# Performance work log

Measured on AMD Instinct MI355X. Metric: run time of the kernel, lower is better.

## Reference

```python
import jax, jax.numpy as jnp
import numpy as np

N_GRAPH = 100000
N_CAND = 10
N_TOTAL = N_GRAPH + N_CAND
F_IN = 128
N_TYPES = 10
E = 6400000


def _p(key, shape, scale=0.05):
    return scale * jax.random.normal(key, shape, dtype=jnp.float32)


def setup_inputs() -> dict:
    key = jax.random.key(0)
    ks = jax.random.split(key, 20)
    x = jax.random.normal(ks[0], (N_GRAPH, F_IN), dtype=jnp.float32)
    candidate_set = jax.random.normal(ks[1], (N_CAND, F_IN), dtype=jnp.float32)
    edge_index = jax.random.randint(ks[2], (2, E), 0, N_GRAPH, dtype=jnp.int64)
    candidate_idx = jnp.arange(N_GRAPH, N_TOTAL, dtype=jnp.int64)  # candidate nodes appended last
    return {
        "x": x, "candidate_set": candidate_set,
        "edge_index": edge_index, "candidate_idx": candidate_idx,
        "W1": _p(ks[3], (F_IN, 16)), "b1": jnp.zeros((16,), jnp.float32),
        "W2": _p(ks[4], (16, 24)), "b2": jnp.zeros((24,), jnp.float32),
        "W3": _p(ks[5], (24, 32)), "b3": jnp.zeros((32,), jnp.float32),
        "Ws1": _p(ks[6], (32, 16)), "bs1": jnp.zeros((16,), jnp.float32),
        "Ws2": _p(ks[7], (16, N_TYPES)), "bs2": jnp.zeros((N_TYPES,), jnp.float32),
        "We1": _p(ks[8], (32, 24)), "be1": jnp.zeros((24,), jnp.float32),
        "We2": _p(ks[9], (24, N_TYPES)), "be2": jnp.zeros((N_TYPES,), jnp.float32),
    }


def _gcn(h, src, dst, W, b, n):
    # GCNConv: x' = D^{-1/2}(A+I)D^{-1/2} X W + b (self-loops added)
    h = h @ W
    deg = jax.ops.segment_sum(jnp.ones(src.shape, h.dtype), dst, num_segments=n) + 1.0
    dinv = jax.lax.rsqrt(deg)
    msg = h[src] * (dinv[src] * dinv[dst])[:, None]
    out = jax.ops.segment_sum(msg, dst, num_segments=n)
    out = out + h * (dinv * dinv)[:, None]  # self-loop term
    return out + b


def relu6(x):
    return jnp.clip(x, 0.0, 6.0)


def reference(x, candidate_set, edge_index, candidate_idx,
              W1, b1, W2, b2, W3, b3,
              Ws1, bs1, Ws2, bs2, We1, be1, We2, be2):
    n = N_TOTAL
    src, dst = edge_index[0], edge_index[1]
    h = jnp.concatenate([x, candidate_set], axis=0)  # [n, F_IN]
    h = _gcn(h, src, dst, W1, b1, n)
    h = _gcn(h, src, dst, W2, b2, n)
    h = _gcn(h, src, dst, W3, b3, n)  # [n, 32]

    start_probs = jax.nn.softmax(relu6(h @ Ws1 + bs1) @ Ws2 + bs2, axis=0)  # [n, T]
    mask = jnp.ones_like(start_probs).at[candidate_idx].set(0.0)
    start_probs = start_probs * mask
    start_probs = jnp.where(start_probs == 0.0, 1e-10, start_probs)
    k1, k2 = jax.random.split(jax.random.key(42))
    start_node = jax.random.categorical(k1, jnp.log(start_probs), axis=-1)  # [n]

    combined = jnp.concatenate([h, h[start_node]], axis=0)  # [2n, 32]
    end_probs = jax.nn.softmax(relu6(combined @ We1 + be1) @ We2 + be2, axis=0)  # [2n, T]
    end_probs = end_probs.at[start_node].set(0.0)
    end_probs = jnp.where(end_probs == 0.0, 1e-10, end_probs)
    end_node = jax.random.categorical(k2, jnp.log(end_probs), axis=-1)  # [2n]
    return (start_node, end_node, start_probs, end_probs)
```

## Files before the change

kernel.cpp:

```cpp
#include <hip/hip_runtime.h>
#include <stdint.h>

constexpr int N_GRAPH = 100000;
constexpr int N_CANDS = 10;
constexpr int NT      = N_GRAPH + N_CANDS;
constexpr int F_IN    = 128;
constexpr int NTYPES  = 10;
constexpr int NE      = 6400000;

constexpr int CB_SHIFT = 9;
constexpr int CB       = 1 << CB_SHIFT;
constexpr int NBK2     = (NT + CB - 1) / CB;
constexpr int SB       = 512;
constexpr int NMAT     = NBK2 * SB;
constexpr int NSCAN_B  = NMAT / 256;
constexpr int TMPENT_CAP = NE + NMAT * 15 + 16;

#define RNG_VARIANT 0

typedef float f4v __attribute__((ext_vector_type(4)));

__device__ __forceinline__ void tf2x32(uint32_t k0, uint32_t k1, uint32_t x0, uint32_t x1,
                                       uint32_t& o0, uint32_t& o1) {
  const uint32_t ks2 = k0 ^ k1 ^ 0x1BD11BDAu;
  uint32_t v0 = x0 + k0, v1 = x1 + k1;
#define TFR(r) { v0 += v1; v1 = (v1 << (r)) | (v1 >> (32 - (r))); v1 ^= v0; }
  TFR(13) TFR(15) TFR(26) TFR(6)
  v0 += k1;  v1 += ks2 + 1u;
  TFR(17) TFR(29) TFR(16) TFR(24)
  v0 += ks2; v1 += k0 + 2u;
  TFR(13) TFR(15) TFR(26) TFR(6)
  v0 += k0;  v1 += k1 + 3u;
  TFR(17) TFR(29) TFR(16) TFR(24)
  v0 += k1;  v1 += ks2 + 4u;
  TFR(13) TFR(15) TFR(26) TFR(6)
  v0 += ks2; v1 += k0 + 5u;
#undef TFR
  o0 = v0; o1 = v1;
}

__device__ __forceinline__ void derive_keys(uint32_t& a0, uint32_t& a1,
                                            uint32_t& b0, uint32_t& b1) {
#if RNG_VARIANT == 2
  uint32_t c0, c1, d0, d1;
  tf2x32(0u, 42u, 0u, 2u, c0, c1);
  tf2x32(0u, 42u, 1u, 3u, d0, d1);
  a0 = c0; a1 = d0; b0 = c1; b1 = d1;
#else
  tf2x32(0u, 42u, 0u, 0u, a0, a1);
  tf2x32(0u, 42u, 0u, 1u, b0, b1);
#endif
}

__device__ __forceinline__ uint32_t rng_bits(uint32_t k0, uint32_t k1,
                                             uint32_t idx, uint32_t total) {
#if RNG_VARIANT == 0
  uint32_t o0, o1; tf2x32(k0, k1, 0u, idx, o0, o1); return o0 ^ o1;
#elif RNG_VARIANT == 1
  uint32_t o0, o1; tf2x32(k0, k1, 0u, idx, o0, o1); return o1;
#else
  uint32_t half = total >> 1; uint32_t o0, o1;
  if (idx < half) { tf2x32(k0, k1, idx, idx + half, o0, o1); return o0; }
  tf2x32(k0, k1, idx - half, idx, o0, o1); return o1;
#endif
}

__device__ __forceinline__ double gumbel_from_bits(uint32_t bits) {
  float uf = __uint_as_float((bits >> 9) | 0x3f800000u) - 1.0f;
  uf = fmaxf(1.17549435e-38f, uf + 1.17549435e-38f);
  return -log(-log((double)uf));
}

__device__ __forceinline__ uint32_t encf(float f) {
  uint32_t u = __float_as_uint(f);
  return u ^ ((u & 0x80000000u) ? 0xFFFFFFFFu : 0x80000000u);
}
__device__ __forceinline__ float decf(uint32_t e) {
  uint32_t u = (e & 0x80000000u) ? (e ^ 0x80000000u) : ~e;
  return __uint_as_float(u);
}

__global__ __launch_bounds__(512) void k_bcount(const int* __restrict__ dst,
                                                int* __restrict__ cntmat,
                                                int* __restrict__ cnt) {
  __shared__ int h[NBK2];
  int tid = threadIdx.x, blk = blockIdx.x;
  for (int b = tid; b < NBK2; b += 512) h[b] = 0;
  __syncthreads();
  int per = (NE + SB - 1) / SB;
  int e0 = blk * per, e1 = min(e0 + per, NE);
  for (int e = e0 + tid; e < e1; e += 512) atomicAdd(&h[dst[e] >> CB_SHIFT], 1);
  __syncthreads();
  for (int b = tid; b < NBK2; b += 512) {
    int c = h[b];
    cntmat[b * SB + blk] = (c + 15) & ~15;
    if (c) atomicAdd(&cnt[b], c);
  }
}

__global__ __launch_bounds__(256) void k_s1(int* __restrict__ cmat, int* __restrict__ partial) {
  __shared__ int sm[256];
  int t = blockIdx.x * 256 + threadIdx.x;
  int v = cmat[t];
  sm[threadIdx.x] = v;
  __syncthreads();
  #pragma unroll
  for (int s = 1; s < 256; s <<= 1) {
    int a = (threadIdx.x >= s) ? sm[threadIdx.x - s] : 0;
    __syncthreads();
    sm[threadIdx.x] += a;
    __syncthreads();
  }
  cmat[t] = sm[threadIdx.x] - v;
  if (threadIdx.x == 255) partial[blockIdx.x] = sm[255];
}

__global__ __launch_bounds__(512) void k_s2(int* __restrict__ partial, int* __restrict__ cmat) {
  __shared__ int sm[512];
  int t = threadIdx.x;
  int v = (t < NSCAN_B) ? partial[t] : 0;
  sm[t] = v;
  __syncthreads();
  #pragma unroll
  for (int s = 1; s < 512; s <<= 1) {
    int a = (t >= s) ? sm[t - s] : 0;
    __syncthreads();
    sm[t] += a;
    __syncthreads();
  }
  if (t < NSCAN_B) partial[t] = sm[t] - v;
  if (t == 511) cmat[NMAT] = sm[511];
}

__global__ __launch_bounds__(256) void k_s3(int* __restrict__ cmat, const int* __restrict__ partial) {
  int t = blockIdx.x * 256 + threadIdx.x;
  cmat[t] += partial[blockIdx.x];
}

__global__ __launch_bounds__(256) void k_rowscan(const int* __restrict__ cnt,
                                                 int* __restrict__ rowbase) {
  __shared__ int sm[256];
  int t = threadIdx.x;
  int v = (t < NBK2) ? cnt[t] : 0;
  sm[t] = v;
  __syncthreads();
  #pragma unroll
  for (int s = 1; s < 256; s <<= 1) {
    int a = (t >= s) ? sm[t - s] : 0;
    __syncthreads();
    sm[t] += a;
    __syncthreads();
  }
  if (t < NBK2) rowbase[t] = sm[t] - v;
}

__global__ __launch_bounds__(512) void k_scatter2(const int* __restrict__ src,
                                                  const int* __restrict__ dst,
                                                  const int* __restrict__ cmat,
                                                  uint32_t* __restrict__ tmpent) {
  __shared__ int lcur[NBK2];
  int tid = threadIdx.x, blk = blockIdx.x;
  for (int b = tid; b < NBK2; b += 512) lcur[b] = cmat[b * SB + blk];
  __syncthreads();
  int per = (NE + SB - 1) / SB;
  int e0 = blk * per, e1 = min(e0 + per, NE);
  for (int e = e0 + tid; e < e1; e += 512) {
    int s = src[e], d = dst[e];
    int b = d >> CB_SHIFT;
    int pos = atomicAdd(&lcur[b], 1);
    tmpent[pos] = (uint32_t)s | ((uint32_t)(d & (CB - 1)) << 17);
  }
  __syncthreads();
  for (int b = tid; b < NBK2; b += 512) {
    int p = lcur[b];
    int end = cmat[b * SB + blk + 1];
    for (; p < end; ++p) tmpent[p] = 0xFFFFFFFFu;
  }
}

__global__ __launch_bounds__(512) void k_place(const uint32_t* __restrict__ tmpent,
                                               const int* __restrict__ cmat,
                                               const int* __restrict__ rowbase,
                                               int* __restrict__ rowptr,
                                               float* __restrict__ dinv,
                                               int* __restrict__ col) {
  __shared__ int sdeg[CB];
  __shared__ int sexc[CB];
  __shared__ int sscan[CB];
  int b = blockIdx.x, tid = threadIdx.x;
  sdeg[tid] = 0;
  __syncthreads();
  int r0 = cmat[b * SB], r1 = cmat[(b + 1) * SB];
  for (int e = r0 + tid; e < r1; e += 512) {
    uint32_t v = tmpent[e];
    if (v != 0xFFFFFFFFu) atomicAdd(&sdeg[v >> 17], 1);
  }
  __syncthreads();
  int d = sdeg[tid];
  sscan[tid] = d;
  __syncthreads();
  #pragma unroll
  for (int s = 1; s < CB; s <<= 1) {
    int v = (tid >= s) ? sscan[tid - s] : 0;
    __syncthreads();
    sscan[tid] += v;
    __syncthreads();
  }
  int rb = rowbase[b];
  int incl = rb + sscan[tid];
  sexc[tid] = incl - d;
  int i = b * CB + tid;
  if (i < NT) {
    rowptr[i + 1] = incl;
    dinv[i] = (float)(1.0 / sqrt((double)(d + 1)));
  }
  if (b == 0 && tid == 0) rowptr[0] = 0;
  __syncthreads();
  for (int e = r0 + tid; e < r1; e += 512) {
    uint32_t v = tmpent[e];
    if (v != 0xFFFFFFFFu) {
      int pos = atomicAdd(&sexc[v >> 17], 1);
      col[pos] = (int)(v & 0x1FFFFu);
    }
  }
}

__global__ __launch_bounds__(256) void k_mm1(const float* __restrict__ x, const float* __restrict__ cand,
                                             const float* __restrict__ W, const float* __restrict__ dinv,
                                             float* __restrict__ zlo, float* __restrict__ zhi) {
  int gid = blockIdx.x * 256 + threadIdx.x;
  if (gid >= NT * 4) return;
  int i = gid >> 2, f4 = gid & 3;
  const float* hr = (i < N_GRAPH) ? (x + (size_t)i * F_IN)
                                  : (cand + (size_t)(i - N_GRAPH) * F_IN);
  const float4* h4 = reinterpret_cast<const float4*>(hr);
  const float4* W4 = reinterpret_cast<const float4*>(W);
  double a0 = 0.0, a1 = 0.0, a2 = 0.0, a3 = 0.0;
  #pragma unroll 8
  for (int q = 0; q < 32; ++q) {
    float4 hv = h4[q];
    float4 w0 = W4[(4 * q + 0) * 4 + f4];
    float4 w1 = W4[(4 * q + 1) * 4 + f4];
    float4 w2 = W4[(4 * q + 2) * 4 + f4];
    float4 w3 = W4[(4 * q + 3) * 4 + f4];
    a0 += (double)hv.x * w0.x + (double)hv.y * w1.x + (double)hv.z * w2.x + (double)hv.w * w3.x;
    a1 += (double)hv.x * w0.y + (double)hv.y * w1.y + (double)hv.z * w2.y + (double)hv.w * w3.y;
    a2 += (double)hv.x * w0.z + (double)hv.y * w1.z + (double)hv.z * w2.z + (double)hv.w * w3.z;
    a3 += (double)hv.x * w0.w + (double)hv.y * w1.w + (double)hv.z * w2.w + (double)hv.w * w3.w;
  }
  double di = (double)dinv[i];
  float4 o;
  o.x = (float)(a0 * di); o.y = (float)(a1 * di);
  o.z = (float)(a2 * di); o.w = (float)(a3 * di);
  if (f4 < 2) reinterpret_cast<float4*>(zlo)[(size_t)i * 2 + f4] = o;
  else        reinterpret_cast<float4*>(zhi)[(size_t)i * 2 + (f4 - 2)] = o;
}

template <bool SQ, bool WITHW, int R>
__global__ __launch_bounds__(2 * R) void k_proph(const int* __restrict__ rowptr,
                                                 const int* __restrict__ col,
                                                 const float* __restrict__ zin,
                                                 const float* __restrict__ win,
                                                 const float* __restrict__ dinv,
                                                 float* __restrict__ zout,
                                                 float* __restrict__ wout,
                                                 float* __restrict__ wsout) {
  int i = blockIdx.x * R + threadIdx.y;
  if (i >= NT) return;
  int fx = threadIdx.x;
  const float4* z4 = reinterpret_cast<const float4*>(zin);
  int e0 = rowptr[i], e1 = rowptr[i + 1];
  double a0 = 0.0, a1 = 0.0, a2 = 0.0, a3 = 0.0, wa = 0.0;
  int e = e0;
  for (; e + 8 <= e1; e += 8) {
    int c0 = __builtin_nontemporal_load(col + e);
    int c1 = __builtin_nontemporal_load(col + e + 1);
    int c2 = __builtin_nontemporal_load(col + e + 2);
    int c3 = __builtin_nontemporal_load(col + e + 3);
    int c4 = __builtin_nontemporal_load(col + e + 4);
    int c5 = __builtin_nontemporal_load(col + e + 5);
    int c6 = __builtin_nontemporal_load(col + e + 6);
    int c7 = __builtin_nontemporal_load(col + e + 7);
    float4 v0 = z4[(size_t)c0 * 2 + fx];
    float4 v1 = z4[(size_t)c1 * 2 + fx];
    float4 v2 = z4[(size_t)c2 * 2 + fx];
    float4 v3 = z4[(size_t)c3 * 2 + fx];
    float4 v4 = z4[(size_t)c4 * 2 + fx];
    float4 v5 = z4[(size_t)c5 * 2 + fx];
    float4 v6 = z4[(size_t)c6 * 2 + fx];
    float4 v7 = z4[(size_t)c7 * 2 + fx];
    if (WITHW && fx == 0) {
      wa += (double)win[c0] + (double)win[c1] + (double)win[c2] + (double)win[c3];
      wa += (double)win[c4] + (double)win[c5] + (double)win[c6] + (double)win[c7];
    }
    a0 += (double)v0.x + (double)v1.x + (double)v2.x + (double)v3.x;
    a1 += (double)v0.y + (double)v1.y + (double)v2.y + (double)v3.y;
    a2 += (double)v0.z + (double)v1.z + (double)v2.z + (double)v3.z;
    a3 += (double)v0.w + (double)v1.w + (double)v2.w + (double)v3.w;
    a0 += (double)v4.x + (double)v5.x + (double)v6.x + (double)v7.x;
    a1 += (double)v4.y + (double)v5.y + (double)v6.y + (double)v7.y;
    a2 += (double)v4.z + (double)v5.z + (double)v6.z + (double)v7.z;
    a3 += (double)v4.w + (double)v5.w + (double)v6.w + (double)v7.w;
  }
  for (; e + 4 <= e1; e += 4) {
    int c0 = __builtin_nontemporal_load(col + e);
    int c1 = __builtin_nontemporal_load(col + e + 1);
    int c2 = __builtin_nontemporal_load(col + e + 2);
    int c3 = __builtin_nontemporal_load(col + e + 3);
    float4 v0 = z4[(size_t)c0 * 2 + fx];
    float4 v1 = z4[(size_t)c1 * 2 + fx];
    float4 v2 = z4[(size_t)c2 * 2 + fx];
    float4 v3 = z4[(size_t)c3 * 2 + fx];
    if (WITHW && fx == 0)
      wa += (double)win[c0] + (double)win[c1] + (double)win[c2] + (double)win[c3];
    a0 += (double)v0.x + (double)v1.x + (double)v2.x + (double)v3.x;
    a1 += (double)v0.y + (double)v1.y + (double)v2.y + (double)v3.y;
    a2 += (double)v0.z + (double)v1.z + (double)v2.z + (double)v3.z;
    a3 += (double)v0.w + (double)v1.w + (double)v2.w + (double)v3.w;
  }
  for (; e < e1; ++e) {
    int c = __builtin_nontemporal_load(col + e);
    float4 v = z4[(size_t)c * 2 + fx];
    if (WITHW && fx == 0) wa += (double)win[c];
    a0 += (double)v.x; a1 += (double)v.y; a2 += (double)v.z; a3 += (double)v.w;
  }
  float4 s = z4[(size_t)i * 2 + fx];
  a0 += (double)s.x; a1 += (double)s.y; a2 += (double)s.z; a3 += (double)s.w;
  double di = (double)dinv[i];
  double sc = SQ ? di * di : di;
  f4v o;
  o.x = (float)(sc * a0); o.y = (float)(sc * a1);
  o.z = (float)(sc * a2); o.w = (float)(sc * a3);
  __builtin_nontemporal_store(o, reinterpret_cast<f4v*>(zout) + (size_t)i * 2 + fx);
  if (WITHW && fx == 0) {
    wa += (double)win[i];
    double w = di * wa;
    wout[i]  = (float)w;
    wsout[i] = (float)(di * w);
  }
}

__global__ __launch_bounds__(512) void k_small(const float* __restrict__ W2, const float* __restrict__ b2p,
                                               const float* __restrict__ W3, const float* __restrict__ b1p,
                                               double* __restrict__ M, double* __restrict__ u,
                                               double* __restrict__ v) {
  __shared__ double t[24];
  int tid = threadIdx.x;
  if (tid < 24) {
    double a = 0.0;
    for (int k = 0; k < 16; ++k) a += (double)b1p[k] * (double)W2[k * 24 + tid];
    t[tid] = a;
  }
  if (tid >= 32 && tid < 64) {
    int o = tid - 32;
    double a = 0.0;
    for (int j = 0; j < 24; ++j) a += (double)b2p[j] * (double)W3[j * 32 + o];
    v[o] = a;
  }
  __syncthreads();
  if (tid < 32) {
    double a = 0.0;
    for (int j = 0; j < 24; ++j) a += t[j] * (double)W3[j * 32 + tid];
    u[tid] = a;
  }
  {
    int k = tid >> 5, o = tid & 31;
    double a = 0.0;
    for (int j = 0; j < 24; ++j) a += (double)W2[k * 24 + j] * (double)W3[j * 32 + o];
    M[tid] = a;
  }
}

__global__ __launch_bounds__(256) void k_epi(const float* __restrict__ zlo, const float* __restrict__ zhi,
                                             const float* __restrict__ w1,
                                             const float* __restrict__ w2,
                                             const double* __restrict__ M, const double* __restrict__ u,
                                             const double* __restrict__ v, const float* __restrict__ b3,
                                             float* __restrict__ H) {
  int gid = blockIdx.x * 256 + threadIdx.x;
  if (gid >= NT * 32) return;
  int i = gid >> 5, o = gid & 31;
  const float* zrl = zlo + (size_t)i * 8;
  const float* zrh = zhi + (size_t)i * 8;
  double acc = (double)b3[o] + (double)w2[i] * u[o] + (double)w1[i] * v[o];
  #pragma unroll
  for (int k = 0; k < 8; ++k) acc += (double)zrl[k] * M[k * 32 + o];
  #pragma unroll
  for (int k = 0; k < 8; ++k) acc += (double)zrh[k] * M[(k + 8) * 32 + o];
  H[gid] = (float)acc;
}

template <int HID>
__global__ __launch_bounds__(256) void k_head(const float* __restrict__ H, const int* __restrict__ sn,
                                              int nrows,
                                              const float* __restrict__ Wa, const float* __restrict__ ba,
                                              const float* __restrict__ Wb, const float* __restrict__ bb,
                                              float* __restrict__ logits) {
  int i = blockIdx.x * 256 + threadIdx.x;
  if (i >= nrows) return;
  int row = (i < NT) ? i : sn[i - NT];
  const float* hr = H + (size_t)row * 32;
  float h[32];
  #pragma unroll
  for (int k = 0; k < 32; ++k) h[k] = hr[k];
  double hid[HID];
  for (int j = 0; j < HID; ++j) {
    double a = (double)ba[j];
    #pragma unroll
    for (int k = 0; k < 32; ++k) a += (double)h[k] * (double)Wa[k * HID + j];
    hid[j] = fmin(fmax(a, 0.0), 6.0);
  }
  for (int t = 0; t < NTYPES; ++t) {
    double l = (double)bb[t];
    #pragma unroll
    for (int j = 0; j < HID; ++j) l += hid[j] * (double)Wb[j * NTYPES + t];
    logits[(size_t)i * NTYPES + t] = (float)l;
  }
}

__global__ __launch_bounds__(256) void k_colmax(const float* __restrict__ L, int nrows,
                                                uint32_t* __restrict__ mb) {
  __shared__ float sm[256][NTYPES];
  float m[NTYPES];
  #pragma unroll
  for (int t = 0; t < NTYPES; ++t) m[t] = -3.402823466e38f;
  for (int r = blockIdx.x * 256 + threadIdx.x; r < nrows; r += gridDim.x * 256) {
    #pragma unroll
    for (int t = 0; t < NTYPES; ++t) m[t] = fmaxf(m[t], L[(size_t)r * NTYPES + t]);
  }
  #pragma unroll
  for (int t = 0; t < NTYPES; ++t) sm[threadIdx.x][t] = m[t];
  __syncthreads();
  for (int s = 128; s > 0; s >>= 1) {
    if (threadIdx.x < s)
      for (int t = 0; t < NTYPES; ++t)
        sm[threadIdx.x][t] = fmaxf(sm[threadIdx.x][t], sm[threadIdx.x + s][t]);
    __syncthreads();
  }
  if (threadIdx.x < NTYPES) atomicMax(&mb[threadIdx.x], encf(sm[0][threadIdx.x]));
}

__global__ __launch_bounds__(256) void k_colsum(const float* __restrict__ L, int nrows,
                                                const uint32_t* __restrict__ mb,
                                                double* __restrict__ sums) {
  __shared__ double sm[256][NTYPES];
  float mx[NTYPES];
  #pragma unroll
  for (int t = 0; t < NTYPES; ++t) mx[t] = decf(mb[t]);
  double s[NTYPES];
  #pragma unroll
  for (int t = 0; t < NTYPES; ++t) s[t] = 0.0;
  for (int r = blockIdx.x * 256 + threadIdx.x; r < nrows; r += gridDim.x * 256) {
    #pragma unroll
    for (int t = 0; t < NTYPES; ++t)
      s[t] += exp((double)L[(size_t)r * NTYPES + t] - (double)mx[t]);
  }
  #pragma unroll
  for (int t = 0; t < NTYPES; ++t) sm[threadIdx.x][t] = s[t];
  __syncthreads();
  for (int st = 128; st > 0; st >>= 1) {
    if (threadIdx.x < st)
      for (int t = 0; t < NTYPES; ++t)
        sm[threadIdx.x][t] += sm[threadIdx.x + st][t];
    __syncthreads();
  }
  if (threadIdx.x < NTYPES) atomicAdd(&sums[threadIdx.x], sm[0][threadIdx.x]);
}

__global__ __launch_bounds__(256) void k_probs_start(const float* __restrict__ L,
                                                     const uint32_t* __restrict__ mb,
                                                     const double* __restrict__ sums,
                                                     float* __restrict__ P) {
  int gid = blockIdx.x * 256 + threadIdx.x;
  if (gid >= NT * NTYPES) return;
  int i = gid / NTYPES, t = gid - i * NTYPES;
  double p = exp((double)L[gid] - (double)decf(mb[t])) / sums[t];
  float pf = (float)p;
  if (i >= N_GRAPH || pf == 0.0f) pf = 1e-10f;
  P[gid] = pf;
}

__global__ __launch_bounds__(256) void k_probs_end(const float* __restrict__ L,
                                                   const uint32_t* __restrict__ mb,
                                                   const double* __restrict__ sums,
                                                   const int* __restrict__ flags,
                                                   float* __restrict__ P) {
  int gid = blockIdx.x * 256 + threadIdx.x;
  if (gid >= 2 * NT * NTYPES) return;
  int j = gid / NTYPES, t = gid - j * NTYPES;
  double p = exp((double)L[gid] - (double)decf(mb[t])) / sums[t];
  float pf = (float)p;
  if ((j < NTYPES && flags[j]) || pf == 0.0f) pf = 1e-10f;
  P[gid] = pf;
}

__global__ __launch_bounds__(256) void k_sample_start(const float* __restrict__ probs,
                                                      float* __restrict__ outSN,
                                                      int* __restrict__ sn, int* __restrict__ flags) {
  int i = blockIdx.x * 256 + threadIdx.x;
  if (i >= NT) return;
  uint32_t a0, a1, b0, b1; derive_keys(a0, a1, b0, b1);
  double best = -1e300; int bi = 0;
  #pragma unroll
  for (int t = 0; t < NTYPES; ++t) {
    uint32_t bits = rng_bits(a0, a1, (uint32_t)(i * NTYPES + t), (uint32_t)(NT * NTYPES));
    double v = log((double)probs[(size_t)i * NTYPES + t]) + gumbel_from_bits(bits);
    if (v > best) { best = v; bi = t; }
  }
  sn[i] = bi;
  outSN[i] = (float)bi;
  flags[bi] = 1;
}

__global__ __launch_bounds__(256) void k_sample_end(const float* __restrict__ probs,
                                                    float* __restrict__ outEN) {
  int j = blockIdx.x * 256 + threadIdx.x;
  if (j >= 2 * NT) return;
  uint32_t a0, a1, b0, b1; derive_keys(a0, a1, b0, b1);
  double best = -1e300; int bi = 0;
  #pragma unroll
  for (int t = 0; t < NTYPES; ++t) {
    uint32_t bits = rng_bits(b0, b1, (uint32_t)(j * NTYPES + t), (uint32_t)(2 * NT * NTYPES));
    double v = log((double)probs[(size_t)j * NTYPES + t]) + gumbel_from_bits(bits);
    if (v > best) { best = v; bi = t; }
  }
  outEN[j] = (float)bi;
}

extern "C" void kernel_launch(void* const* d_in, const int* in_sizes, int n_in,
                              void* d_out, int out_size, void* d_ws, size_t ws_size,
                              hipStream_t stream) {
  const float* x    = (const float*)d_in[0];
  const float* cand = (const float*)d_in[1];
  const int*   ei   = (const int*)d_in[2];
  const float* W1 = (const float*)d_in[4];  const float* b1 = (const float*)d_in[5];
  const float* W2 = (const float*)d_in[6];  const float* b2 = (const float*)d_in[7];
  const float* W3 = (const float*)d_in[8];  const float* b3 = (const float*)d_in[9];
  const float* Ws1 = (const float*)d_in[10]; const float* bs1 = (const float*)d_in[11];
  const float* Ws2 = (const float*)d_in[12]; const float* bs2 = (const float*)d_in[13];
  const float* We1 = (const float*)d_in[14]; const float* be1 = (const float*)d_in[15];
  const float* We2 = (const float*)d_in[16]; const float* be2 = (const float*)d_in[17];
  float* out = (float*)d_out;
  float* outSN = out;
  float* outEN = out + NT;
  float* outPS = out + 3 * NT;
  float* outPE = out + 13 * NT;

  char* ws = (char*)d_ws;
  size_t off = 0;
  auto alloc = [&](size_t bytes) -> void* {
    void* p = ws + off;
    off += (bytes + 511) & ~(size_t)511;
    return p;
  };
  float*    dinv    = (float*)alloc((size_t)NT * 4);
  int*      rowptr  = (int*)alloc((size_t)(NT + 1) * 4);
  int*      cnt     = (int*)alloc((size_t)NBK2 * 4);
  int*      rowbase = (int*)alloc((size_t)NBK2 * 4);
  int*      cmat    = (int*)alloc((size_t)(NMAT + 1) * 4);
  int*      partial = (int*)alloc(512 * 4);
  int*      col     = (int*)alloc((size_t)NE * 4);
  char*     ublk    = (char*)alloc((size_t)TMPENT_CAP * 4);
  uint32_t* tmpent  = (uint32_t*)ublk;
  float*    zloA    = (float*)ublk;
  float*    zhiA    = (float*)(ublk + (size_t)NT * 8 * 4);
  float*    zloB    = (float*)(ublk + (size_t)NT * 8 * 4 * 2);
  float*    zhiB    = (float*)(ublk + (size_t)NT * 8 * 4 * 3);
  float*    Ha      = (float*)(ublk + (size_t)NT * 8 * 4 * 4);
  float*    logitsS = (float*)alloc((size_t)NT * NTYPES * 4);
  float*    logitsE = (float*)alloc((size_t)2 * NT * NTYPES * 4);
  float*    w1v     = (float*)alloc((size_t)NT * 4);
  float*    ws1v    = (float*)alloc((size_t)NT * 4);
  float*    w2v     = (float*)alloc((size_t)NT * 4);
  float*    wsd     = (float*)alloc((size_t)NT * 4);
  double*   Md      = (double*)alloc(512 * 8);
  double*   ud      = (double*)alloc(32 * 8);
  double*   vd      = (double*)alloc(32 * 8);
  int*      sn      = (int*)alloc((size_t)NT * 4);
  uint32_t* maxS    = (uint32_t*)alloc(64);
  double*   sumS    = (double*)alloc(128);
  uint32_t* maxE    = (uint32_t*)alloc(64);
  double*   sumE    = (double*)alloc(128);
  int*      flags   = (int*)alloc(64);
  (void)ws_size; (void)in_sizes; (void)n_in; (void)out_size;

  const int* srcA = ei;
  const int* dstA = ei + NE;

  const int B = 256;
  auto blocks = [](long long nthreads) { return (int)((nthreads + 255) / 256); };

  hipMemsetAsync(cnt, 0, (size_t)NBK2 * 4, stream);
  k_bcount<<<SB, 512, 0, stream>>>(dstA, cmat, cnt);
  k_s1<<<NSCAN_B, 256, 0, stream>>>(cmat, partial);
  k_s2<<<1, 512, 0, stream>>>(partial, cmat);
  k_s3<<<NSCAN_B, 256, 0, stream>>>(cmat, partial);
  k_rowscan<<<1, 256, 0, stream>>>(cnt, rowbase);
  k_scatter2<<<SB, 512, 0, stream>>>(srcA, dstA, cmat, tmpent);
  k_place<<<NBK2, 512, 0, stream>>>(tmpent, cmat, rowbase, rowptr, dinv, col);

  k_small<<<1, 512, 0, stream>>>(W2, b2, W3, b1, Md, ud, vd);
  k_mm1<<<blocks((long long)NT * 4), B, 0, stream>>>(x, cand, W1, dinv, zloA, zhiA);
  const int PR = 128, PBLK = (NT + PR - 1) / PR;
  k_proph<true,  true,  PR><<<PBLK, dim3(2, PR), 0, stream>>>(rowptr, col, zloA, dinv, dinv, zloB, w1v, ws1v);
  k_proph<true,  false, PR><<<PBLK, dim3(2, PR), 0, stream>>>(rowptr, col, zhiA, nullptr, dinv, zhiB, nullptr, nullptr);
  k_proph<true,  true,  PR><<<PBLK, dim3(2, PR), 0, stream>>>(rowptr, col, zloB, ws1v, dinv, zloA, w2v, wsd);
  k_proph<true,  false, PR><<<PBLK, dim3(2, PR), 0, stream>>>(rowptr, col, zhiB, nullptr, dinv, zhiA, nullptr, nullptr);
  k_proph<false, false, PR><<<PBLK, dim3(2, PR), 0, stream>>>(rowptr, col, zloA, nullptr, dinv, zloB, nullptr, nullptr);
  k_proph<false, false, PR><<<PBLK, dim3(2, PR), 0, stream>>>(rowptr, col, zhiA, nullptr, dinv, zhiB, nullptr, nullptr);
  k_epi<<<blocks((long long)NT * 32), B, 0, stream>>>(zloB, zhiB, w1v, w2v, Md, ud, vd, b3, Ha);

  k_head<16><<<blocks(NT), B, 0, stream>>>(Ha, sn, NT, Ws1, bs1, Ws2, bs2, logitsS);
  hipMemsetAsync(maxS, 0, (size_t)((char*)flags - (char*)maxS) + 512, stream);
  k_colmax<<<512, B, 0, stream>>>(logitsS, NT, maxS);
  k_colsum<<<512, B, 0, stream>>>(logitsS, NT, maxS, sumS);
  k_probs_start<<<blocks((long long)NT * NTYPES), B, 0, stream>>>(logitsS, maxS, sumS, outPS);
  k_sample_start<<<blocks(NT), B, 0, stream>>>(outPS, outSN, sn, flags);

  k_head<24><<<blocks(2 * NT), B, 0, stream>>>(Ha, sn, 2 * NT, We1, be1, We2, be2, logitsE);
  k_colmax<<<512, B, 0, stream>>>(logitsE, 2 * NT, maxE);
  k_colsum<<<512, B, 0, stream>>>(logitsE, 2 * NT, maxE, sumE);
  k_probs_end<<<blocks((long long)2 * NT * NTYPES), B, 0, stream>>>(logitsE, maxE, sumE, flags, outPE);
  k_sample_end<<<blocks(2 * NT), B, 0, stream>>>(outPE, outEN);
}
```

Baseline: 965.1 us.

## Merge lo/hi propagation passes into one XCD-aware kernel with edge splitting

Replaces the six per-half SpMM propagation launches with three launches. Each launch handles both 8-float halves of the feature vector, and blocks are mapped by XCD so that one group of XCDs reads only one half, which keeps that half's working set in the local L2. Each row now uses two edge-splitting lanes per float4, combined by a shuffle reduction, to add memory-level parallelism. In exchange the 8-wide unroll is dropped and the shuffle adds overhead, and the block-to-XCD mapping assumes the hardware assigns blocks round-robin across 8 XCDs.

```diff
diff --git a/kernel.cpp b/kernel.cpp
--- a/kernel.cpp
+++ b/kernel.cpp
@@ -257,52 +257,31 @@
 }
 
 template <bool SQ, bool WITHW, int R>
-__global__ __launch_bounds__(2 * R) void k_proph(const int* __restrict__ rowptr,
-                                                 const int* __restrict__ col,
-                                                 const float* __restrict__ zin,
-                                                 const float* __restrict__ win,
-                                                 const float* __restrict__ dinv,
-                                                 float* __restrict__ zout,
-                                                 float* __restrict__ wout,
-                                                 float* __restrict__ wsout) {
-  int i = blockIdx.x * R + threadIdx.y;
+__global__ __launch_bounds__(4 * R, 6) void k_prop2(const int* __restrict__ rowptr,
+                                                    const int* __restrict__ col,
+                                                    const float* __restrict__ zin,
+                                                    const float* __restrict__ win,
+                                                    const float* __restrict__ dinv,
+                                                    float* __restrict__ zout,
+                                                    float* __restrict__ wout,
+                                                    float* __restrict__ wsout) {
+  int bid = blockIdx.x;
+  int xcd  = bid & 7;
+  int g    = bid >> 3;
+  int half = xcd >> 2;
+  int sub  = (g << 2) | (xcd & 3);
+  int i = sub * R + threadIdx.y;
   if (i >= NT) return;
-  int fx = threadIdx.x;
-  const float4* z4 = reinterpret_cast<const float4*>(zin);
+  int fx = threadIdx.x & 1;
+  int es = threadIdx.x >> 1;
+  const float4* z4 = reinterpret_cast<const float4*>(zin + (size_t)half * NT * 8);
   int e0 = rowptr[i], e1 = rowptr[i + 1];
+  int len = e1 - e0;
+  int ngrp = len >> 2;
   double a0 = 0.0, a1 = 0.0, a2 = 0.0, a3 = 0.0, wa = 0.0;
-  int e = e0;
-  for (; e + 8 <= e1; e += 8) {
-    int c0 = __builtin_nontemporal_load(col + e);
-    int c1 = __builtin_nontemporal_load(col + e + 1);
-    int c2 = __builtin_nontemporal_load(col + e + 2);
-    int c3 = __builtin_nontemporal_load(col + e + 3);
-    int c4 = __builtin_nontemporal_load(col + e + 4);
-    int c5 = __builtin_nontemporal_load(col + e + 5);
-    int c6 = __builtin_nontemporal_load(col + e + 6);
-    int c7 = __builtin_nontemporal_load(col + e + 7);
-    float4 v0 = z4[(size_t)c0 * 2 + fx];
-    float4 v1 = z4[(size_t)c1 * 2 + fx];
-    float4 v2 = z4[(size_t)c2 * 2 + fx];
-    float4 v3 = z4[(size_t)c3 * 2 + fx];
-    float4 v4 = z4[(size_t)c4 * 2 + fx];
-    float4 v5 = z4[(size_t)c5 * 2 + fx];
-    float4 v6 = z4[(size_t)c6 * 2 + fx];
-    float4 v7 = z4[(size_t)c7 * 2 + fx];
-    if (WITHW && fx == 0) {
-      wa += (double)win[c0] + (double)win[c1] + (double)win[c2] + (double)win[c3];
-      wa += (double)win[c4] + (double)win[c5] + (double)win[c6] + (double)win[c7];
-    }
-    a0 += (double)v0.x + (double)v1.x + (double)v2.x + (double)v3.x;
-    a1 += (double)v0.y + (double)v1.y + (double)v2.y + (double)v3.y;
-    a2 += (double)v0.z + (double)v1.z + (double)v2.z + (double)v3.z;
-    a3 += (double)v0.w + (double)v1.w + (double)v2.w + (double)v3.w;
-    a0 += (double)v4.x + (double)v5.x + (double)v6.x + (double)v7.x;
-    a1 += (double)v4.y + (double)v5.y + (double)v6.y + (double)v7.y;
-    a2 += (double)v4.z + (double)v5.z + (double)v6.z + (double)v7.z;
-    a3 += (double)v4.w + (double)v5.w + (double)v6.w + (double)v7.w;
-  }
-  for (; e + 4 <= e1; e += 4) {
+  const bool dow = WITHW && (half == 0) && (fx == 0);
+  for (int gq = es; gq < ngrp; gq += 2) {
+    int e = e0 + (gq << 2);
     int c0 = __builtin_nontemporal_load(col + e);
     int c1 = __builtin_nontemporal_load(col + e + 1);
     int c2 = __builtin_nontemporal_load(col + e + 2);
@@ -311,32 +290,41 @@
     float4 v1 = z4[(size_t)c1 * 2 + fx];
     float4 v2 = z4[(size_t)c2 * 2 + fx];
     float4 v3 = z4[(size_t)c3 * 2 + fx];
-    if (WITHW && fx == 0)
+    if (dow)
       wa += (double)win[c0] + (double)win[c1] + (double)win[c2] + (double)win[c3];
     a0 += (double)v0.x + (double)v1.x + (double)v2.x + (double)v3.x;
     a1 += (double)v0.y + (double)v1.y + (double)v2.y + (double)v3.y;
     a2 += (double)v0.z + (double)v1.z + (double)v2.z + (double)v3.z;
     a3 += (double)v0.w + (double)v1.w + (double)v2.w + (double)v3.w;
   }
-  for (; e < e1; ++e) {
-    int c = __builtin_nontemporal_load(col + e);
-    float4 v = z4[(size_t)c * 2 + fx];
-    if (WITHW && fx == 0) wa += (double)win[c];
-    a0 += (double)v.x; a1 += (double)v.y; a2 += (double)v.z; a3 += (double)v.w;
-  }
-  float4 s = z4[(size_t)i * 2 + fx];
-  a0 += (double)s.x; a1 += (double)s.y; a2 += (double)s.z; a3 += (double)s.w;
-  double di = (double)dinv[i];
-  double sc = SQ ? di * di : di;
-  f4v o;
-  o.x = (float)(sc * a0); o.y = (float)(sc * a1);
-  o.z = (float)(sc * a2); o.w = (float)(sc * a3);
-  __builtin_nontemporal_store(o, reinterpret_cast<f4v*>(zout) + (size_t)i * 2 + fx);
-  if (WITHW && fx == 0) {
-    wa += (double)win[i];
-    double w = di * wa;
-    wout[i]  = (float)w;
-    wsout[i] = (float)(di * w);
+  if (es == (ngrp & 1)) {
+    for (int e = e0 + (ngrp << 2); e < e1; ++e) {
+      int c = __builtin_nontemporal_load(col + e);
+      float4 v = z4[(size_t)c * 2 + fx];
+      if (dow) wa += (double)win[c];
+      a0 += (double)v.x; a1 += (double)v.y; a2 += (double)v.z; a3 += (double)v.w;
+    }
+  }
+  a0 += __shfl_xor(a0, 2);
+  a1 += __shfl_xor(a1, 2);
+  a2 += __shfl_xor(a2, 2);
+  a3 += __shfl_xor(a3, 2);
+  if (WITHW) wa += __shfl_xor(wa, 2);
+  if (es == 0) {
+    float4 s = z4[(size_t)i * 2 + fx];
+    a0 += (double)s.x; a1 += (double)s.y; a2 += (double)s.z; a3 += (double)s.w;
+    double di = (double)dinv[i];
+    double sc = SQ ? di * di : di;
+    f4v o;
+    o.x = (float)(sc * a0); o.y = (float)(sc * a1);
+    o.z = (float)(sc * a2); o.w = (float)(sc * a3);
+    __builtin_nontemporal_store(o, reinterpret_cast<f4v*>(zout + (size_t)half * NT * 8) + (size_t)i * 2 + fx);
+    if (dow) {
+      wa += (double)win[i];
+      double w = di * wa;
+      wout[i]  = (float)w;
+      wsout[i] = (float)(di * w);
+    }
   }
 }
 
@@ -562,10 +550,8 @@
   int*      col     = (int*)alloc((size_t)NE * 4);
   char*     ublk    = (char*)alloc((size_t)TMPENT_CAP * 4);
   uint32_t* tmpent  = (uint32_t*)ublk;
-  float*    zloA    = (float*)ublk;
-  float*    zhiA    = (float*)(ublk + (size_t)NT * 8 * 4);
-  float*    zloB    = (float*)(ublk + (size_t)NT * 8 * 4 * 2);
-  float*    zhiB    = (float*)(ublk + (size_t)NT * 8 * 4 * 3);
+  float*    zA      = (float*)ublk;
+  float*    zB      = (float*)(ublk + (size_t)NT * 8 * 4 * 2);
   float*    Ha      = (float*)(ublk + (size_t)NT * 8 * 4 * 4);
   float*    logitsS = (float*)alloc((size_t)NT * NTYPES * 4);
   float*    logitsE = (float*)alloc((size_t)2 * NT * NTYPES * 4);
@@ -600,15 +586,14 @@
   k_place<<<NBK2, 512, 0, stream>>>(tmpent, cmat, rowbase, rowptr, dinv, col);
 
   k_small<<<1, 512, 0, stream>>>(W2, b2, W3, b1, Md, ud, vd);
-  k_mm1<<<blocks((long long)NT * 4), B, 0, stream>>>(x, cand, W1, dinv, zloA, zhiA);
-  const int PR = 128, PBLK = (NT + PR - 1) / PR;
-  k_proph<true,  true,  PR><<<PBLK, dim3(2, PR), 0, stream>>>(rowptr, col, zloA, dinv, dinv, zloB, w1v, ws1v);
-  k_proph<true,  false, PR><<<PBLK, dim3(2, PR), 0, stream>>>(rowptr, col, zhiA, nullptr, dinv, zhiB, nullptr, nullptr);
-  k_proph<true,  true,  PR><<<PBLK, dim3(2, PR), 0, stream>>>(rowptr, col, zloB, ws1v, dinv, zloA, w2v, wsd);
-  k_proph<true,  false, PR><<<PBLK, dim3(2, PR), 0, stream>>>(rowptr, col, zhiB, nullptr, dinv, zhiA, nullptr, nullptr);
-  k_proph<false, false, PR><<<PBLK, dim3(2, PR), 0, stream>>>(rowptr, col, zloA, nullptr, dinv, zloB, nullptr, nullptr);
-  k_proph<false, false, PR><<<PBLK, dim3(2, PR), 0, stream>>>(rowptr, col, zhiA, nullptr, dinv, zhiB, nullptr, nullptr);
-  k_epi<<<blocks((long long)NT * 32), B, 0, stream>>>(zloB, zhiB, w1v, w2v, Md, ud, vd, b3, Ha);
+  k_mm1<<<blocks((long long)NT * 4), B, 0, stream>>>(x, cand, W1, dinv, zA, zA + (size_t)NT * 8);
+  const int PR2  = 64;
+  const int NSUB = (NT + PR2 - 1) / PR2;
+  const int PNB  = (((NSUB + 3) & ~3) * 2);
+  k_prop2<true,  true,  PR2><<<PNB, dim3(4, PR2), 0, stream>>>(rowptr, col, zA, dinv, dinv, zB, w1v, ws1v);
+  k_prop2<true,  true,  PR2><<<PNB, dim3(4, PR2), 0, stream>>>(rowptr, col, zB, ws1v, dinv, zA, w2v, wsd);
+  k_prop2<false, false, PR2><<<PNB, dim3(4, PR2), 0, stream>>>(rowptr, col, zA, nullptr, dinv, zB, nullptr, nullptr);
+  k_epi<<<blocks((long long)NT * 32), B, 0, stream>>>(zB, zB + (size_t)NT * 8, w1v, w2v, Md, ud, vd, b3, Ha);
 
   k_head<16><<<blocks(NT), B, 0, stream>>>(Ha, sn, NT, Ws1, bs1, Ws2, bs2, logitsS);
   hipMemsetAsync(maxS, 0, (size_t)((char*)flags - (char*)maxS) + 512, stream);
```

After: 950.3 us. Within noise of the previous version (-1.5%).
